# Kernel tuning notes

Hardware: AMD Instinct MI355X
Metric: run time of the kernel (lower is better)

Reference implementation:

```python
import jax, jax.numpy as jnp
import numpy as np

N_POINTS = 2_000_000
GRID = 256  # voxel grid resolution (D=H=W), production-scale stand-in for source's 128


def setup_inputs() -> dict:
    key = jax.random.key(0)
    k1, k2, k3 = jax.random.split(key, 3)
    coords = jax.random.uniform(k1, (N_POINTS, 3), dtype=jnp.float32,
                                minval=-0.95, maxval=0.95)
    registration_pred = jax.random.normal(k2, (N_POINTS, 3), dtype=jnp.float32) * 0.02
    registration_gt = jax.random.normal(k3, (N_POINTS, 3), dtype=jnp.float32) * 0.02
    return {"registration_pred": registration_pred,
            "registration_gt": registration_gt,
            "coords": coords}


def _splat(pts, size):
    """Trilinear scatter (adjoint of F.grid_sample, align_corners=False,
    zero padding). pts: [N,3] normalized coords in (x,y,z) order mapping to
    (W,H,D). Splats weight 1 per point. Returns [D,H,W] volume."""
    D = H = W = size
    # grid_sample align_corners=False unnormalization: p = ((g+1)*size - 1)/2
    x = ((pts[:, 0] + 1.0) * W - 1.0) * 0.5
    y = ((pts[:, 1] + 1.0) * H - 1.0) * 0.5
    z = ((pts[:, 2] + 1.0) * D - 1.0) * 0.5
    x0f, y0f, z0f = jnp.floor(x), jnp.floor(y), jnp.floor(z)
    fx, fy, fz = x - x0f, y - y0f, z - z0f  # fractional offsets
    x0, y0, z0 = x0f.astype(jnp.int32), y0f.astype(jnp.int32), z0f.astype(jnp.int32)
    vol = jnp.zeros(D * H * W, dtype=pts.dtype)
    for dz in (0, 1):
        wz = fz if dz else (1.0 - fz)
        for dy in (0, 1):
            wy = fy if dy else (1.0 - fy)
            for dx in (0, 1):
                wx = fx if dx else (1.0 - fx)
                xi, yi, zi = x0 + dx, y0 + dy, z0 + dz
                valid = ((xi >= 0) & (xi < W) & (yi >= 0) & (yi < H)
                         & (zi >= 0) & (zi < D))
                w = jnp.where(valid, wx * wy * wz, 0.0)
                idx = jnp.where(valid, (zi * H + yi) * W + xi, 0)
                vol = vol.at[idx].add(w)
    return vol.reshape(D, H, W)


def reference(registration_pred, registration_gt, coords):
    pred_vol = _splat(coords + registration_pred, GRID)
    gt_vol = _splat(coords + registration_gt, GRID)
    # HuberLoss(reduction='sum', delta=1.0)
    d = pred_vol - gt_vol
    ad = jnp.abs(d)
    return jnp.sum(jnp.where(ad <= 1.0, 0.5 * d * d, ad - 0.5))
```

## Files before the change

### kernel.cpp

```cpp
#include <hip/hip_runtime.h>

#define GRID_RES 256
#define NCELLS 1024
#define NB 1024
#define BCAP 6144
#define NPT 2
#define ISEGCAP 5888

#define W_SCALE 2097152.0f
#define INV_W (1.0f / 2097152.0f)
#define L_SCALE 512.0f
#define INV_L (1.0f / 512.0f)

struct CEv { unsigned w0, w1q, xyz; };

__device__ __forceinline__ CEv make_cev(float px, float py, float pz,
                                        unsigned sign) {
    float x = ((px + 1.0f) * (float)GRID_RES - 1.0f) * 0.5f;
    float y = ((py + 1.0f) * (float)GRID_RES - 1.0f) * 0.5f;
    float z = ((pz + 1.0f) * (float)GRID_RES - 1.0f) * 0.5f;
    float xf = floorf(x), yf = floorf(y), zf = floorf(z);
    int x0 = (int)xf, y0 = (int)yf, z0 = (int)zf;
    unsigned qx = (unsigned)((x - xf) * 65535.0f + 0.5f);
    unsigned qy = (unsigned)((y - yf) * 65535.0f + 0.5f);
    unsigned qz = (unsigned)((z - zf) * 16383.0f + 0.5f);
    bool valid = (x0 >= -1) & (x0 <= 255) & (y0 >= -1) & (y0 <= 255) &
                 (z0 >= -1) & (z0 <= 255);
    CEv e;
    e.w0 = qx | (qy << 16);
    e.w1q = qz | (sign << 31);
    e.xyz = valid ? ((unsigned)(x0 + 1) | ((unsigned)(y0 + 1) << 10) |
                     ((unsigned)(z0 + 1) << 20) | (1u << 30))
                  : 0u;
    return e;
}

template <typename F>
__device__ __forceinline__ void enum_cells(const CEv& e, F&& emit) {
    if (!(e.xyz & (1u << 30))) return;
    int x0 = (int)(e.xyz & 1023u) - 1;
    int y0 = (int)((e.xyz >> 10) & 1023u) - 1;
    int z0 = (int)((e.xyz >> 20) & 1023u) - 1;
    int cxs[2], cys[2], czs[2];
    int nx = 0, ny = 0, nz = 0;
    {
        bool vA = (x0 >= 0) & (x0 <= 255);
        bool vB = (x0 >= -1) & (x0 <= 254);
        int cA = x0 >> 5, cB = (x0 + 1) >> 5;
        if (vA) cxs[nx++] = cA;
        if (vB && (!vA || cB != cA)) cxs[nx++] = cB;
    }
    {
        bool vA = (y0 >= 0) & (y0 <= 255);
        bool vB = (y0 >= -1) & (y0 <= 254);
        int cA = y0 >> 5, cB = (y0 + 1) >> 5;
        if (vA) cys[ny++] = cA;
        if (vB && (!vA || cB != cA)) cys[ny++] = cB;
    }
    {
        bool vA = (z0 >= 0) & (z0 <= 255);
        bool vB = (z0 >= -1) & (z0 <= 254);
        int cA = z0 >> 4, cB = (z0 + 1) >> 4;
        if (vA) czs[nz++] = cA;
        if (vB && (!vA || cB != cA)) czs[nz++] = cB;
    }
    for (int a = 0; a < nz; ++a) {
        int cz = czs[a];
        unsigned lz = (unsigned)(z0 - (cz << 4) + 1);
        for (int b = 0; b < ny; ++b) {
            int cy = cys[b];
            unsigned ly = (unsigned)(y0 - (cy << 5) + 1);
            for (int c = 0; c < nx; ++c) {
                int cx = cxs[c];
                unsigned lx = (unsigned)(x0 - (cx << 5) + 1);
                int cell = (cz << 6) | (cy << 3) | cx;
                unsigned w1 = e.w1q | (lx << 14) | (ly << 20) | (lz << 26);
                emit(cell, e.w0, w1);
            }
        }
    }
}

__global__ __launch_bounds__(1024) void bin_kernel(
    const float* __restrict__ pred, const float* __restrict__ gt,
    const float* __restrict__ coords, unsigned* __restrict__ segTab,
    uint2* __restrict__ payload, int* __restrict__ lossAcc, int n) {
    __shared__ unsigned h[NCELLS];
    __shared__ unsigned wtot[16];
    __shared__ unsigned totalS;
    __shared__ uint4 plq[BCAP / 2];
    uint2* pl = (uint2*)plq;
    int b = blockIdx.x;
    int t = threadIdx.x;
    if (b == 0 && t == 0) lossAcc[0] = 0;
    h[t] = 0;
    __syncthreads();

    int chunk = (n + NB - 1) / NB;
    int start = b * chunk;
    int end = min(start + chunk, n);
    const float3* c3 = (const float3*)coords;
    const float3* p3 = (const float3*)pred;
    const float3* g3 = (const float3*)gt;

    CEv ev[2 * NPT];
#pragma unroll
    for (int k = 0; k < NPT; ++k) {
        int i = start + t + (k << 10);
        if (i < end) {
            float3 c = c3[i];
            float3 p = p3[i];
            float3 g = g3[i];
            ev[2 * k] = make_cev(c.x + p.x, c.y + p.y, c.z + p.z, 0u);
            ev[2 * k + 1] = make_cev(c.x + g.x, c.y + g.y, c.z + g.z, 1u);
        } else {
            ev[2 * k].xyz = 0;
            ev[2 * k + 1].xyz = 0;
        }
    }

#pragma unroll
    for (int k = 0; k < 2 * NPT; ++k)
        enum_cells(ev[k], [&](int cell, unsigned, unsigned) {
            atomicAdd(&h[cell], 1u);
        });
    __syncthreads();

    unsigned x = h[t];
    unsigned incl = x;
    int lane = t & 63, wid = t >> 6;
#pragma unroll
    for (int off = 1; off < 64; off <<= 1) {
        unsigned y = __shfl_up(incl, off, 64);
        if (lane >= off) incl += y;
    }
    if (lane == 63) wtot[wid] = incl;
    __syncthreads();
    if (t == 0) {
        unsigned r = 0;
#pragma unroll
        for (int w = 0; w < 16; ++w) { unsigned v = wtot[w]; wtot[w] = r; r += v; }
        totalS = r;
    }
    __syncthreads();
    unsigned offE = incl - x + wtot[wid];
    segTab[(size_t)b * NCELLS + t] = (offE << 16) | x;
    h[t] = offE;
    __syncthreads();

#pragma unroll
    for (int k = 0; k < 2 * NPT; ++k)
        enum_cells(ev[k], [&](int cell, unsigned w0, unsigned w1) {
            unsigned slot = atomicAdd(&h[cell], 1u);
            if (slot < (unsigned)BCAP) pl[slot] = make_uint2(w0, w1);
        });
    __syncthreads();

    unsigned tot = totalS;
    unsigned m = min((tot + 1u) >> 1, (unsigned)(BCAP / 2));
    uint4* gp4 = (uint4*)(payload + (size_t)b * BCAP);
    for (unsigned i = t; i < m; i += 1024) gp4[i] = plq[i];
}

__global__ __launch_bounds__(1024) void accum_kernel(
    const uint2* __restrict__ payload, const unsigned* __restrict__ segTab,
    int* __restrict__ lossAcc) {
    __shared__ int4 v4s[4096];
    __shared__ unsigned short itemSeg[ISEGCAP];
    __shared__ unsigned pbs[NB];
    __shared__ unsigned w16[16];
    __shared__ float wsum[16];
    __shared__ unsigned totalS;
    int* v = (int*)v4s;
    int c = blockIdx.x;
    int t = threadIdx.x;
    int4 z; z.x = 0; z.y = 0; z.z = 0; z.w = 0;
#pragma unroll
    for (int j = 0; j < 4; ++j) v4s[t + (j << 10)] = z;

    unsigned tab = segTab[(size_t)t * NCELLS + c];
    unsigned cnt = tab & 0xFFFFu;
    unsigned off = tab >> 16;
    int lane = t & 63, wid = t >> 6;
    unsigned incl = cnt;
#pragma unroll
    for (int o = 1; o < 64; o <<= 1) {
        unsigned y = __shfl_up(incl, o, 64);
        if (lane >= o) incl += y;
    }
    if (lane == 63) w16[wid] = incl;
    __syncthreads();
    if (t == 0) {
        unsigned r = 0;
#pragma unroll
        for (int w = 0; w < 16; ++w) { unsigned q = w16[w]; w16[w] = r; r += q; }
        totalS = r;
    }
    __syncthreads();
    unsigned base = incl - cnt + w16[wid];
    pbs[t] = (unsigned)t * (unsigned)BCAP + off - base;
    for (unsigned k = 0; k < cnt; ++k) {
        unsigned idx = base + k;
        if (idx < (unsigned)ISEGCAP) itemSeg[idx] = (unsigned short)t;
    }
    __syncthreads();

    unsigned total = min(totalS, (unsigned)ISEGCAP);
    for (unsigned i = t; i < total; i += 1024) {
        unsigned seg = itemSeg[i];
        uint2 p = payload[(size_t)(unsigned)(pbs[seg] + i)];
        float fx = (float)(p.x & 0xFFFFu) * (1.0f / 65535.0f);
        float fy = (float)(p.x >> 16) * (1.0f / 65535.0f);
        float fz = (float)(p.y & 0x3FFFu) * (1.0f / 16383.0f);
        int lx = (int)((p.y >> 14) & 63u);
        int ly = (int)((p.y >> 20) & 63u);
        int lz = (int)((p.y >> 26) & 31u);
        float s = (p.y >> 31) ? -W_SCALE : W_SCALE;
        float wxs[2] = {1.0f - fx, fx};
        float wys[2] = {1.0f - fy, fy};
        float wzs[2] = {1.0f - fz, fz};
        int xb = lx - 1, yb = ly - 1, zb = lz - 1;
#pragma unroll
        for (int dz = 0; dz < 2; ++dz) {
            int rz = zb + dz;
            if ((unsigned)rz > 15u) continue;
            float wz = s * wzs[dz];
#pragma unroll
            for (int dy = 0; dy < 2; ++dy) {
                int ry = yb + dy;
                if ((unsigned)ry > 31u) continue;
                float wyz = wz * wys[dy];
#pragma unroll
                for (int dx = 0; dx < 2; ++dx) {
                    int rx = xb + dx;
                    if ((unsigned)rx > 31u) continue;
                    int iw = __float2int_rn(wyz * wxs[dx]);
                    atomicAdd(&v[(rz << 10) | (ry << 5) | rx], iw);
                }
            }
        }
    }
    __syncthreads();

    float acc = 0.0f;
#pragma unroll
    for (int j = 0; j < 4; ++j) {
        int4 q = v4s[t + (j << 10)];
        {
            float d = (float)q.x * INV_W;
            float ad = fabsf(d);
            acc += (ad <= 1.0f) ? 0.5f * d * d : ad - 0.5f;
        }
        {
            float d = (float)q.y * INV_W;
            float ad = fabsf(d);
            acc += (ad <= 1.0f) ? 0.5f * d * d : ad - 0.5f;
        }
        {
            float d = (float)q.z * INV_W;
            float ad = fabsf(d);
            acc += (ad <= 1.0f) ? 0.5f * d * d : ad - 0.5f;
        }
        {
            float d = (float)q.w * INV_W;
            float ad = fabsf(d);
            acc += (ad <= 1.0f) ? 0.5f * d * d : ad - 0.5f;
        }
    }
#pragma unroll
    for (int o = 32; o > 0; o >>= 1) acc += __shfl_down(acc, o, 64);
    if (lane == 0) wsum[wid] = acc;
    __syncthreads();
    if (t == 0) {
        float tsum = 0.0f;
#pragma unroll
        for (int w = 0; w < 16; ++w) tsum += wsum[w];
        atomicAdd(lossAcc, __float2int_rn(tsum * L_SCALE));
    }
}

__global__ void finalize_kernel(const int* __restrict__ lossAcc,
                                float* __restrict__ out) {
    out[0] = (float)lossAcc[0] * INV_L;
}

extern "C" void kernel_launch(void* const* d_in, const int* in_sizes, int n_in,
                              void* d_out, int out_size, void* d_ws, size_t ws_size,
                              hipStream_t stream) {
    const float* reg_pred = (const float*)d_in[0];
    const float* reg_gt   = (const float*)d_in[1];
    const float* coords   = (const float*)d_in[2];
    float* out = (float*)d_out;

    char* ws = (char*)d_ws;
    int* lossAcc = (int*)ws;
    unsigned* segTab = (unsigned*)(ws + 256);
    uint2* payload = (uint2*)(ws + 256 + (size_t)NB * NCELLS * 4);

    int n = in_sizes[0] / 3;

    bin_kernel<<<NB, 1024, 0, stream>>>(reg_pred, reg_gt, coords, segTab,
                                        payload, lossAcc, n);
    accum_kernel<<<NCELLS, 1024, 0, stream>>>(payload, segTab, lossAcc);
    finalize_kernel<<<1, 1, 0, stream>>>(lossAcc, out);
}
```

Before: 156.3 us.

## Batch payload loads, simplify cell enumeration, fuse finalize into accumulate kernel

Replaces the per-event cell enumeration with lo/hi range loops, hoists the segTab load ahead of shared-memory zeroing, and unrolls the accumulate loop into six items whose global loads are issued before any atomics. It also removes the separate finalize kernel: the last accumulate block, found through a done counter with thread fences, writes the output. The aim is more memory-level parallelism and one fewer launch, at the cost of extra registers and a global atomic counter.

```diff
diff --git a/kernel.cpp b/kernel.cpp
--- a/kernel.cpp
+++ b/kernel.cpp
@@ -35,56 +35,31 @@
     return e;
 }
 
-template <typename F>
-__device__ __forceinline__ void enum_cells(const CEv& e, F&& emit) {
-    if (!(e.xyz & (1u << 30))) return;
-    int x0 = (int)(e.xyz & 1023u) - 1;
-    int y0 = (int)((e.xyz >> 10) & 1023u) - 1;
-    int z0 = (int)((e.xyz >> 20) & 1023u) - 1;
-    int cxs[2], cys[2], czs[2];
-    int nx = 0, ny = 0, nz = 0;
-    {
-        bool vA = (x0 >= 0) & (x0 <= 255);
-        bool vB = (x0 >= -1) & (x0 <= 254);
-        int cA = x0 >> 5, cB = (x0 + 1) >> 5;
-        if (vA) cxs[nx++] = cA;
-        if (vB && (!vA || cB != cA)) cxs[nx++] = cB;
-    }
-    {
-        bool vA = (y0 >= 0) & (y0 <= 255);
-        bool vB = (y0 >= -1) & (y0 <= 254);
-        int cA = y0 >> 5, cB = (y0 + 1) >> 5;
-        if (vA) cys[ny++] = cA;
-        if (vB && (!vA || cB != cA)) cys[ny++] = cB;
-    }
-    {
-        bool vA = (z0 >= 0) & (z0 <= 255);
-        bool vB = (z0 >= -1) & (z0 <= 254);
-        int cA = z0 >> 4, cB = (z0 + 1) >> 4;
-        if (vA) czs[nz++] = cA;
-        if (vB && (!vA || cB != cA)) czs[nz++] = cB;
-    }
-    for (int a = 0; a < nz; ++a) {
-        int cz = czs[a];
-        unsigned lz = (unsigned)(z0 - (cz << 4) + 1);
-        for (int b = 0; b < ny; ++b) {
-            int cy = cys[b];
-            unsigned ly = (unsigned)(y0 - (cy << 5) + 1);
-            for (int c = 0; c < nx; ++c) {
-                int cx = cxs[c];
-                unsigned lx = (unsigned)(x0 - (cx << 5) + 1);
-                int cell = (cz << 6) | (cy << 3) | cx;
-                unsigned w1 = e.w1q | (lx << 14) | (ly << 20) | (lz << 26);
-                emit(cell, e.w0, w1);
-            }
-        }
-    }
+__device__ __forceinline__ bool ev_decode(const CEv& e, int& x0, int& y0,
+                                          int& z0, int& xlo, int& xhi,
+                                          int& ylo, int& yhi, int& zlo,
+                                          int& zhi) {
+    if (!(e.xyz & (1u << 30))) return false;
+    x0 = (int)(e.xyz & 1023u) - 1;
+    y0 = (int)((e.xyz >> 10) & 1023u) - 1;
+    z0 = (int)((e.xyz >> 20) & 1023u) - 1;
+    int cax = x0 >> 5, cbx = (x0 + 1) >> 5;
+    xlo = (x0 >= 0) ? cax : cbx;
+    xhi = (x0 <= 254) ? cbx : cax;
+    int cay = y0 >> 5, cby = (y0 + 1) >> 5;
+    ylo = (y0 >= 0) ? cay : cby;
+    yhi = (y0 <= 254) ? cby : cay;
+    int caz = z0 >> 4, cbz = (z0 + 1) >> 4;
+    zlo = (z0 >= 0) ? caz : cbz;
+    zhi = (z0 <= 254) ? cbz : caz;
+    return true;
 }
 
 __global__ __launch_bounds__(1024) void bin_kernel(
     const float* __restrict__ pred, const float* __restrict__ gt,
     const float* __restrict__ coords, unsigned* __restrict__ segTab,
-    uint2* __restrict__ payload, int* __restrict__ lossAcc, int n) {
+    uint2* __restrict__ payload, int* __restrict__ lossAcc,
+    unsigned* __restrict__ doneCnt, int n) {
     __shared__ unsigned h[NCELLS];
     __shared__ unsigned wtot[16];
     __shared__ unsigned totalS;
@@ -92,7 +67,10 @@
     uint2* pl = (uint2*)plq;
     int b = blockIdx.x;
     int t = threadIdx.x;
-    if (b == 0 && t == 0) lossAcc[0] = 0;
+    if (b == 0 && t == 0) {
+        lossAcc[0] = 0;
+        doneCnt[0] = 0;
+    }
     h[t] = 0;
     __syncthreads();
 
@@ -120,10 +98,17 @@
     }
 
 #pragma unroll
-    for (int k = 0; k < 2 * NPT; ++k)
-        enum_cells(ev[k], [&](int cell, unsigned, unsigned) {
-            atomicAdd(&h[cell], 1u);
-        });
+    for (int k = 0; k < 2 * NPT; ++k) {
+        int x0, y0, z0, xlo, xhi, ylo, yhi, zlo, zhi;
+        if (ev_decode(ev[k], x0, y0, z0, xlo, xhi, ylo, yhi, zlo, zhi)) {
+            for (int cz = zlo; cz <= zhi; ++cz)
+                for (int cy = ylo; cy <= yhi; ++cy) {
+                    int cyz = (cz << 6) | (cy << 3);
+                    for (int cx = xlo; cx <= xhi; ++cx)
+                        atomicAdd(&h[cyz | cx], 1u);
+                }
+        }
+    }
     __syncthreads();
 
     unsigned x = h[t];
@@ -149,11 +134,25 @@
     __syncthreads();
 
 #pragma unroll
-    for (int k = 0; k < 2 * NPT; ++k)
-        enum_cells(ev[k], [&](int cell, unsigned w0, unsigned w1) {
-            unsigned slot = atomicAdd(&h[cell], 1u);
-            if (slot < (unsigned)BCAP) pl[slot] = make_uint2(w0, w1);
-        });
+    for (int k = 0; k < 2 * NPT; ++k) {
+        int x0, y0, z0, xlo, xhi, ylo, yhi, zlo, zhi;
+        if (ev_decode(ev[k], x0, y0, z0, xlo, xhi, ylo, yhi, zlo, zhi)) {
+            unsigned w0 = ev[k].w0, w1q = ev[k].w1q;
+            for (int cz = zlo; cz <= zhi; ++cz) {
+                unsigned wz = w1q | ((unsigned)(z0 - (cz << 4) + 1) << 26);
+                for (int cy = ylo; cy <= yhi; ++cy) {
+                    unsigned wzy = wz | ((unsigned)(y0 - (cy << 5) + 1) << 20);
+                    int cyz = (cz << 6) | (cy << 3);
+                    for (int cx = xlo; cx <= xhi; ++cx) {
+                        unsigned w1 =
+                            wzy | ((unsigned)(x0 - (cx << 5) + 1) << 14);
+                        unsigned slot = atomicAdd(&h[cyz | cx], 1u);
+                        if (slot < (unsigned)BCAP) pl[slot] = make_uint2(w0, w1);
+                    }
+                }
+            }
+        }
+    }
     __syncthreads();
 
     unsigned tot = totalS;
@@ -162,9 +161,43 @@
     for (unsigned i = t; i < m; i += 1024) gp4[i] = plq[i];
 }
 
+__device__ __forceinline__ void accum_item(uint2 p, int* v) {
+    float fx = (float)(p.x & 0xFFFFu) * (1.0f / 65535.0f);
+    float fy = (float)(p.x >> 16) * (1.0f / 65535.0f);
+    float fz = (float)(p.y & 0x3FFFu) * (1.0f / 16383.0f);
+    int lx = (int)((p.y >> 14) & 63u);
+    int ly = (int)((p.y >> 20) & 63u);
+    int lz = (int)((p.y >> 26) & 31u);
+    float s = (p.y >> 31) ? -W_SCALE : W_SCALE;
+    float wxs[2] = {1.0f - fx, fx};
+    float wys[2] = {1.0f - fy, fy};
+    float wzs[2] = {1.0f - fz, fz};
+    int xb = lx - 1, yb = ly - 1, zb = lz - 1;
+#pragma unroll
+    for (int dz = 0; dz < 2; ++dz) {
+        int rz = zb + dz;
+        if ((unsigned)rz > 15u) continue;
+        float wz = s * wzs[dz];
+#pragma unroll
+        for (int dy = 0; dy < 2; ++dy) {
+            int ry = yb + dy;
+            if ((unsigned)ry > 31u) continue;
+            float wyz = wz * wys[dy];
+#pragma unroll
+            for (int dx = 0; dx < 2; ++dx) {
+                int rx = xb + dx;
+                if ((unsigned)rx > 31u) continue;
+                int iw = __float2int_rn(wyz * wxs[dx]);
+                atomicAdd(&v[(rz << 10) | (ry << 5) | rx], iw);
+            }
+        }
+    }
+}
+
 __global__ __launch_bounds__(1024) void accum_kernel(
     const uint2* __restrict__ payload, const unsigned* __restrict__ segTab,
-    int* __restrict__ lossAcc) {
+    int* __restrict__ lossAcc, unsigned* __restrict__ doneCnt,
+    float* __restrict__ out) {
     __shared__ int4 v4s[4096];
     __shared__ unsigned short itemSeg[ISEGCAP];
     __shared__ unsigned pbs[NB];
@@ -174,11 +207,11 @@
     int* v = (int*)v4s;
     int c = blockIdx.x;
     int t = threadIdx.x;
+    unsigned tab = segTab[(size_t)t * NCELLS + c];
     int4 z; z.x = 0; z.y = 0; z.z = 0; z.w = 0;
 #pragma unroll
     for (int j = 0; j < 4; ++j) v4s[t + (j << 10)] = z;
 
-    unsigned tab = segTab[(size_t)t * NCELLS + c];
     unsigned cnt = tab & 0xFFFFu;
     unsigned off = tab >> 16;
     int lane = t & 63, wid = t >> 6;
@@ -206,40 +239,23 @@
     __syncthreads();
 
     unsigned total = min(totalS, (unsigned)ISEGCAP);
-    for (unsigned i = t; i < total; i += 1024) {
-        unsigned seg = itemSeg[i];
-        uint2 p = payload[(size_t)(unsigned)(pbs[seg] + i)];
-        float fx = (float)(p.x & 0xFFFFu) * (1.0f / 65535.0f);
-        float fy = (float)(p.x >> 16) * (1.0f / 65535.0f);
-        float fz = (float)(p.y & 0x3FFFu) * (1.0f / 16383.0f);
-        int lx = (int)((p.y >> 14) & 63u);
-        int ly = (int)((p.y >> 20) & 63u);
-        int lz = (int)((p.y >> 26) & 31u);
-        float s = (p.y >> 31) ? -W_SCALE : W_SCALE;
-        float wxs[2] = {1.0f - fx, fx};
-        float wys[2] = {1.0f - fy, fy};
-        float wzs[2] = {1.0f - fz, fz};
-        int xb = lx - 1, yb = ly - 1, zb = lz - 1;
-#pragma unroll
-        for (int dz = 0; dz < 2; ++dz) {
-            int rz = zb + dz;
-            if ((unsigned)rz > 15u) continue;
-            float wz = s * wzs[dz];
-#pragma unroll
-            for (int dy = 0; dy < 2; ++dy) {
-                int ry = yb + dy;
-                if ((unsigned)ry > 31u) continue;
-                float wyz = wz * wys[dy];
-#pragma unroll
-                for (int dx = 0; dx < 2; ++dx) {
-                    int rx = xb + dx;
-                    if ((unsigned)rx > 31u) continue;
-                    int iw = __float2int_rn(wyz * wxs[dx]);
-                    atomicAdd(&v[(rz << 10) | (ry << 5) | rx], iw);
-                }
-            }
-        }
-    }
+    unsigned i0 = (unsigned)t, i1 = i0 + 1024, i2 = i0 + 2048, i3 = i0 + 3072,
+             i4 = i0 + 4096, i5 = i0 + 5120;
+    bool b0 = i0 < total, b1 = i1 < total, b2 = i2 < total, b3 = i3 < total,
+         b4 = i4 < total, b5 = i5 < total;
+    uint2 p0 = make_uint2(0, 0), p1 = p0, p2 = p0, p3 = p0, p4 = p0, p5 = p0;
+    if (b0) p0 = payload[(size_t)(unsigned)(pbs[itemSeg[i0]] + i0)];
+    if (b1) p1 = payload[(size_t)(unsigned)(pbs[itemSeg[i1]] + i1)];
+    if (b2) p2 = payload[(size_t)(unsigned)(pbs[itemSeg[i2]] + i2)];
+    if (b3) p3 = payload[(size_t)(unsigned)(pbs[itemSeg[i3]] + i3)];
+    if (b4) p4 = payload[(size_t)(unsigned)(pbs[itemSeg[i4]] + i4)];
+    if (b5) p5 = payload[(size_t)(unsigned)(pbs[itemSeg[i5]] + i5)];
+    if (b0) accum_item(p0, v);
+    if (b1) accum_item(p1, v);
+    if (b2) accum_item(p2, v);
+    if (b3) accum_item(p3, v);
+    if (b4) accum_item(p4, v);
+    if (b5) accum_item(p5, v);
     __syncthreads();
 
     float acc = 0.0f;
@@ -276,12 +292,14 @@
 #pragma unroll
         for (int w = 0; w < 16; ++w) tsum += wsum[w];
         atomicAdd(lossAcc, __float2int_rn(tsum * L_SCALE));
-    }
-}
-
-__global__ void finalize_kernel(const int* __restrict__ lossAcc,
-                                float* __restrict__ out) {
-    out[0] = (float)lossAcc[0] * INV_L;
+        __threadfence();
+        unsigned done = atomicAdd(doneCnt, 1u);
+        if (done == (unsigned)(NCELLS - 1)) {
+            __threadfence();
+            int lv = atomicAdd(lossAcc, 0);
+            out[0] = (float)lv * INV_L;
+        }
+    }
 }
 
 extern "C" void kernel_launch(void* const* d_in, const int* in_sizes, int n_in,
@@ -294,13 +312,14 @@
 
     char* ws = (char*)d_ws;
     int* lossAcc = (int*)ws;
+    unsigned* doneCnt = (unsigned*)(ws + 64);
     unsigned* segTab = (unsigned*)(ws + 256);
     uint2* payload = (uint2*)(ws + 256 + (size_t)NB * NCELLS * 4);
 
     int n = in_sizes[0] / 3;
 
     bin_kernel<<<NB, 1024, 0, stream>>>(reg_pred, reg_gt, coords, segTab,
-                                        payload, lossAcc, n);
-    accum_kernel<<<NCELLS, 1024, 0, stream>>>(payload, segTab, lossAcc);
-    finalize_kernel<<<1, 1, 0, stream>>>(lossAcc, out);
-}
+                                        payload, lossAcc, doneCnt, n);
+    accum_kernel<<<NCELLS, 1024, 0, stream>>>(payload, segTab, lossAcc,
+                                              doneCnt, out);
+}
```

New measurement: 178.6 us. 1.14x slower.
